# Kernel tuning notes

Measured on AMD Instinct MI355X. Metric: run time of the kernel, lower is better.

Reference implementation:

```python
import jax, jax.numpy as jnp
import numpy as np

K = 9
SIGMA = 4.0
RADIUS = 16  # round(4*sigma)
IMAGE_SHAPE = (256, 256)


def _gaussian_kernel_1d():
    i = jnp.arange(2 * RADIUS + 1, dtype=jnp.float32) - RADIUS
    g = jnp.exp(-(i ** 2) / (2.0 * SIGMA ** 2))
    return g / jnp.sum(g)


def _gaussian_blur(x):
    # x: [b, H, W, 1]; separable Gaussian blur, reflect-101 borders (cv2 default)
    g = _gaussian_kernel_1d()
    xp = jnp.pad(x, ((0, 0), (RADIUS, RADIUS), (RADIUS, RADIUS), (0, 0)), mode='reflect')
    dn = ('NHWC', 'HWIO', 'NHWC')
    kv = g.reshape(2 * RADIUS + 1, 1, 1, 1)  # vertical pass
    kh = g.reshape(1, 2 * RADIUS + 1, 1, 1)  # horizontal pass
    y = jax.lax.conv_general_dilated(xp, kv, (1, 1), 'VALID', dimension_numbers=dn)
    y = jax.lax.conv_general_dilated(y, kh, (1, 1), 'VALID', dimension_numbers=dn)
    return y


def setup_inputs() -> dict:
    key = jax.random.key(0)
    k1, k2 = jax.random.split(key)
    inputs = jax.random.normal(k1, (8, 32, 32, 512), dtype=jnp.float32)
    feature_vector = jax.random.normal(k2, (16384, 512), dtype=jnp.float32)
    return {"inputs": inputs, "feature_vector": feature_vector}


def reference(inputs, feature_vector):
    b, h, w, c = inputs.shape
    feat = inputs.reshape(b * h * w, c)
    # pairwise euclidean distances: [b*h*w, N]
    d2 = (jnp.sum(feat ** 2, axis=-1, keepdims=True)
          + jnp.sum(feature_vector ** 2, axis=-1)[None, :]
          - 2.0 * feat @ feature_vector.T)
    dist = jnp.sqrt(jnp.maximum(d2, 0.0))
    # k smallest distances, ascending (equivalent to tf.sort(...)[..., :k])
    neg_topk, _ = jax.lax.top_k(-dist, K)
    score = -neg_topk  # [b*h*w, K], ascending
    mask = score[:, 0].reshape(b, h, w, 1)
    score = score.reshape(b, h * w, K)
    # patch with maximal nearest-neighbor distance
    idx = jnp.argmax(score[..., 0], axis=-1)  # [b]
    conf = jnp.take_along_axis(score, idx[:, None, None], axis=1)[:, 0, :]  # [b, K]
    exp_conf = jnp.exp(conf)
    weight = 1.0 - jnp.max(exp_conf, axis=-1) / jnp.sum(exp_conf, axis=-1)
    score_out = (jnp.max(score[..., 0], axis=-1) * weight)[:, None]  # [b, 1]
    mask = jax.image.resize(mask, (b, *IMAGE_SHAPE, 1), method='bilinear', antialias=False)
    mask = _gaussian_blur(mask)
    return score_out, mask
```

## Files before the change

kernel.cpp:

```cpp
#include <hip/hip_runtime.h>

typedef __attribute__((ext_vector_type(8))) short bf16x8;
typedef __attribute__((ext_vector_type(4))) float f32x4;

static constexpr int M = 8192;
static constexpr int N = 16384;
static constexpr int K = 512;
static constexpr int BM = 256;
static constexpr int BN = 256;
static constexpr int RBLK = M / BM;
static constexpr int CBLK = N / BN;
static constexpr int BMs = 128;
static constexpr int BKs = 64;
static constexpr int KCHUNKS_S = K / BKs;
static constexpr int NGROUPS_S = 8;
static constexpr int GROUP_N_S = N / NGROUPS_S;
static constexpr int NTILES_S = GROUP_N_S / 128;
static constexpr float F_INF = 3.0e38f;

__device__ __forceinline__ unsigned short f2bf(float f) {
    unsigned int u = __float_as_uint(f);
    return (unsigned short)((u + 0x7fffu + ((u >> 16) & 1u)) >> 16);
}

__device__ __forceinline__ void gl_lds16(const void* g, void* l) {
    __builtin_amdgcn_global_load_lds(
        (const __attribute__((address_space(1))) unsigned int*)g,
        (__attribute__((address_space(3))) unsigned int*)l, 16, 0, 0);
}

__global__ void k_prep(const float* __restrict__ Q, const float* __restrict__ F,
                       unsigned short* __restrict__ Qb, unsigned short* __restrict__ Fb,
                       float* __restrict__ qn, float* __restrict__ fn) {
    int wid = blockIdx.x * 4 + (threadIdx.x >> 6);
    int lane = threadIdx.x & 63;
    bool isQ = wid < M;
    const float* src = isQ ? (Q + (size_t)wid * K) : (F + (size_t)(wid - M) * K);
    unsigned short* dst = isQ ? (Qb + (size_t)wid * K) : (Fb + (size_t)(wid - M) * K);
    const float4* p = reinterpret_cast<const float4*>(src) + lane * 2;
    float4 a = p[0], b = p[1];
    float s = a.x*a.x + a.y*a.y + a.z*a.z + a.w*a.w
            + b.x*b.x + b.y*b.y + b.z*b.z + b.w*b.w;
    bf16x8 v;
    v[0]=(short)f2bf(a.x); v[1]=(short)f2bf(a.y); v[2]=(short)f2bf(a.z); v[3]=(short)f2bf(a.w);
    v[4]=(short)f2bf(b.x); v[5]=(short)f2bf(b.y); v[6]=(short)f2bf(b.z); v[7]=(short)f2bf(b.w);
    *reinterpret_cast<bf16x8*>(dst + lane * 8) = v;
    #pragma unroll
    for (int d = 1; d < 64; d <<= 1) s += __shfl_xor(s, d);
    if (lane == 0) { if (isQ) qn[wid] = s; else fn[wid - M] = s; }
}

__global__ void k_norms(const float* __restrict__ Q, const float* __restrict__ F,
                        float* __restrict__ qn, float* __restrict__ fn) {
    int wid = blockIdx.x * 4 + (threadIdx.x >> 6);
    int lane = threadIdx.x & 63;
    const float* src = (wid < M) ? (Q + (size_t)wid * K) : (F + (size_t)(wid - M) * K);
    const float4* p = reinterpret_cast<const float4*>(src) + lane * 2;
    float4 a = p[0], b = p[1];
    float s = a.x*a.x + a.y*a.y + a.z*a.z + a.w*a.w
            + b.x*b.x + b.y*b.y + b.z*b.z + b.w*b.w;
    #pragma unroll
    for (int d = 1; d < 64; d <<= 1) s += __shfl_xor(s, d);
    if (lane == 0) { if (wid < M) qn[wid] = s; else fn[wid - M] = s; }
}

__global__ __launch_bounds__(512, 1)
void k_mingemm9(const unsigned short* __restrict__ Qb, const unsigned short* __restrict__ Fb,
                const float* __restrict__ qn, const float* __restrict__ fn,
                float* __restrict__ pv, unsigned int* __restrict__ pi) {
    __shared__ unsigned short As[2][2][8192];
    __shared__ unsigned short Bs[2][2][8192];
    __shared__ float redv[256][4];
    __shared__ unsigned int redi[256][4];

    const int tid = threadIdx.x;
    const int lane = tid & 63;
    const int wave = tid >> 6;
    const int wr = wave >> 2;
    const int wc = wave & 3;
    const int l15 = lane & 15, l4 = lane >> 4, l7 = lane & 7;
    const int r3 = lane >> 3;
    const int g8 = (lane & 7) ^ r3;

    const int wg = blockIdx.x;
    const int x = wg & 7, q = wg >> 3;
    const int c_blk = x * 8 + (q & 7);
    const int r_blk = q >> 3;
    const int row0 = r_blk * BM;
    const int col0 = c_blk * BN;

#define STAGE_A(t, hh) do {                                                        \
    _Pragma("unroll")                                                              \
    for (int i = 0; i < 2; ++i)                                                    \
        gl_lds16(Qb + (size_t)(row0 + (hh)*128 + i*64 + wave*8 + r3) * K           \
                    + (t)*64 + g8*8,                                               \
                 &As[(t)&1][hh][(i*64 + wave*8) * 64]);                            \
} while (0)
#define STAGE_B(t, hh) do {                                                        \
    _Pragma("unroll")                                                              \
    for (int i = 0; i < 2; ++i)                                                    \
        gl_lds16(Fb + (size_t)(col0 + (hh)*128 + i*64 + wave*8 + r3) * K           \
                    + (t)*64 + g8*8,                                               \
                 &Bs[(t)&1][hh][(i*64 + wave*8) * 64]);                            \
} while (0)

    f32x4 acc[8][4];
    #pragma unroll
    for (int a = 0; a < 8; ++a)
        #pragma unroll
        for (int b = 0; b < 4; ++b) acc[a][b] = f32x4{0.f, 0.f, 0.f, 0.f};

    bf16x8 afr[4][2], bfr[4][2];

#define PHASE(t, s, STMT, VMN) do {                                                \
    if ((s) == 0) {                                                                \
        _Pragma("unroll")                                                          \
        for (int f = 0; f < 4; ++f)                                                \
            _Pragma("unroll")                                                      \
            for (int ks = 0; ks < 2; ++ks)                                         \
                afr[f][ks] = *reinterpret_cast<const bf16x8*>(                     \
                    &As[(t)&1][wr][(f*16 + l15)*64 + (((ks*4 + l4) ^ l7))*8]);     \
        _Pragma("unroll")                                                          \
        for (int f = 0; f < 2; ++f)                                                \
            _Pragma("unroll")                                                      \
            for (int ks = 0; ks < 2; ++ks)                                         \
                bfr[f][ks] = *reinterpret_cast<const bf16x8*>(                     \
                    &Bs[(t)&1][0][(wc*32 + f*16 + l15)*64 + (((ks*4 + l4) ^ l7))*8]); \
    } else if ((s) == 1) {                                                         \
        _Pragma("unroll")                                                          \
        for (int f = 0; f < 2; ++f)                                                \
            _Pragma("unroll")                                                      \
            for (int ks = 0; ks < 2; ++ks)                                         \
                bfr[2 + f][ks] = *reinterpret_cast<const bf16x8*>(                 \
                    &Bs[(t)&1][1][(wc*32 + f*16 + l15)*64 + (((ks*4 + l4) ^ l7))*8]); \
    } else if ((s) == 2) {                                                         \
        _Pragma("unroll")                                                          \
        for (int f = 0; f < 4; ++f)                                                \
            _Pragma("unroll")                                                      \
            for (int ks = 0; ks < 2; ++ks)                                         \
                afr[f][ks] = *reinterpret_cast<const bf16x8*>(                     \
                    &As[(t)&1][wr][((f+4)*16 + l15)*64 + (((ks*4 + l4) ^ l7))*8]); \
    }                                                                              \
    STMT;                                                                          \
    __builtin_amdgcn_s_setprio(1);                                                 \
    {                                                                              \
        const int AB = ((s) >= 2) ? 4 : 0;                                         \
        const int FJ = ((s) & 1) ? 2 : 0;                                          \
        _Pragma("unroll")                                                          \
        for (int f = 0; f < 4; ++f)                                                \
            _Pragma("unroll")                                                      \
            for (int j2 = 0; j2 < 2; ++j2)                                         \
                _Pragma("unroll")                                                  \
                for (int ks = 0; ks < 2; ++ks)                                     \
                    acc[AB + f][FJ + j2] = __builtin_amdgcn_mfma_f32_16x16x32_bf16(\
                        afr[f][ks], bfr[FJ + j2][ks], acc[AB + f][FJ + j2], 0,0,0);\
    }                                                                              \
    __builtin_amdgcn_s_setprio(0);                                                 \
    asm volatile("s_waitcnt vmcnt(" #VMN ")" ::: "memory");                        \
    __builtin_amdgcn_s_barrier();                                                  \
    __builtin_amdgcn_sched_barrier(0);                                             \
} while (0)

    STAGE_B(0, 0); STAGE_B(0, 1); STAGE_A(0, 0); STAGE_A(0, 1);
    STAGE_B(1, 0); STAGE_B(1, 1); STAGE_A(1, 0);
    asm volatile("s_waitcnt vmcnt(6)" ::: "memory");
    __builtin_amdgcn_s_barrier();
    __builtin_amdgcn_sched_barrier(0);

#define ITER(T)                                        \
    PHASE(T,     0, STAGE_A((T)+1, 1), 6);             \
    PHASE(T,     1, STAGE_B((T)+2, 0), 6);             \
    PHASE(T,     2, STAGE_B((T)+2, 1), 6);             \
    PHASE(T,     3, STAGE_A((T)+2, 0), 6);             \
    PHASE((T)+1, 0, STAGE_A((T)+2, 1), 6);             \
    PHASE((T)+1, 1, STAGE_B((T)+3, 0), 6);             \
    PHASE((T)+1, 2, STAGE_B((T)+3, 1), 6);             \
    PHASE((T)+1, 3, STAGE_A((T)+3, 0), 6);

    ITER(0)
    ITER(2)
    ITER(4)
    PHASE(6, 0, STAGE_A(7, 1), 6);
    PHASE(6, 1, (void)0, 6);
    PHASE(6, 2, (void)0, 6);
    PHASE(6, 3, (void)0, 0);
    PHASE(7, 0, (void)0, 0);
    PHASE(7, 1, (void)0, 0);
    PHASE(7, 2, (void)0, 0);
    PHASE(7, 3, (void)0, 0);
#undef ITER
#undef PHASE
#undef STAGE_A
#undef STAGE_B

    float fnv[4];
    int colg[4];
    #pragma unroll
    for (int fj = 0; fj < 4; ++fj) {
        colg[fj] = col0 + (fj < 2 ? wc*32 + fj*16 : 128 + wc*32 + (fj - 2)*16) + l15;
        fnv[fj] = fn[colg[fj]];
    }
    #pragma unroll
    for (int fi = 0; fi < 8; ++fi) {
        #pragma unroll
        for (int j = 0; j < 4; ++j) {
            int rloc = wr*128 + fi*16 + l4*4 + j;
            float qv = qn[row0 + rloc];
            float v = F_INF; unsigned int ix = 0;
            #pragma unroll
            for (int fj = 0; fj < 4; ++fj) {
                float d2 = qv + fnv[fj] - 2.0f * acc[fi][fj][j];
                if (d2 < v) { v = d2; ix = (unsigned int)colg[fj]; }
            }
            #pragma unroll
            for (int d = 1; d < 16; d <<= 1) {
                float ov = __shfl_xor(v, d);
                unsigned int oi = (unsigned int)__shfl_xor((int)ix, d);
                if (ov < v) { v = ov; ix = oi; }
            }
            if (l15 == 0) { redv[rloc][wc] = v; redi[rloc][wc] = ix; }
        }
    }
    __syncthreads();
    if (tid < BM) {
        float v = redv[tid][0]; unsigned int ix = redi[tid][0];
        #pragma unroll
        for (int w2 = 1; w2 < 4; ++w2) {
            float ov = redv[tid][w2];
            if (ov < v) { v = ov; ix = redi[tid][w2]; }
        }
        pv[(size_t)(row0 + tid) * CBLK + c_blk] = v;
        pi[(size_t)(row0 + tid) * CBLK + c_blk] = ix;
    }
}

__global__ __launch_bounds__(256, 2)
void k_mingemm_cast(const float* __restrict__ Q, const float* __restrict__ F,
                    const float* __restrict__ qn, const float* __restrict__ fn,
                    float* __restrict__ pv, unsigned int* __restrict__ pi) {
    __shared__ unsigned short As[BMs * BKs];
    __shared__ unsigned short Bs[BMs * BKs];
    __shared__ float qn_t[BMs];
    __shared__ float fn_t[BMs];

    const int tid = threadIdx.x;
    const int lane = tid & 63;
    const int wave = tid >> 6;
    const int wr = wave >> 1, wc = wave & 1;
    const int l15 = lane & 15, l4 = lane >> 4;

    const int row0 = blockIdx.x * BMs;
    const int gbase = blockIdx.y * GROUP_N_S;

    const int srow = tid >> 3;
    const int p8 = tid & 7;
    const int g8 = p8 ^ (srow & 7);
    const float* pA[4];
    const float* pB[4];
    int dstOff[4];
    #pragma unroll
    for (int i = 0; i < 4; ++i) {
        int r = i * 32 + srow;
        pA[i] = Q + (size_t)(row0 + r) * K + g8 * 8;
        pB[i] = F + (size_t)(gbase + r) * K + g8 * 8;
        dstOff[i] = r * BKs + p8 * 8;
    }

    float mval[4][4];
    unsigned int midx[4][4];
    float qnv[4][4];
    #pragma unroll
    for (int a = 0; a < 4; ++a)
        #pragma unroll
        for (int b = 0; b < 4; ++b) { mval[a][b] = F_INF; midx[a][b] = 0; qnv[a][b] = 0.f; }

    for (int nt = 0; nt < NTILES_S; ++nt) {
        f32x4 acc[4][4];
        #pragma unroll
        for (int a = 0; a < 4; ++a)
            #pragma unroll
            for (int b = 0; b < 4; ++b) acc[a][b] = f32x4{0.f, 0.f, 0.f, 0.f};

        for (int kc = 0; kc < KCHUNKS_S; ++kc) {
            __syncthreads();
            #pragma unroll
            for (int i = 0; i < 4; ++i) {
                const float4* sa = reinterpret_cast<const float4*>(pA[i] + kc * BKs);
                float4 xa = sa[0], ya = sa[1];
                const float4* sb = reinterpret_cast<const float4*>(pB[i] + nt * (128 * K) + kc * BKs);
                float4 xb = sb[0], yb = sb[1];
                bf16x8 va, vb;
                va[0]=(short)f2bf(xa.x); va[1]=(short)f2bf(xa.y); va[2]=(short)f2bf(xa.z); va[3]=(short)f2bf(xa.w);
                va[4]=(short)f2bf(ya.x); va[5]=(short)f2bf(ya.y); va[6]=(short)f2bf(ya.z); va[7]=(short)f2bf(ya.w);
                vb[0]=(short)f2bf(xb.x); vb[1]=(short)f2bf(xb.y); vb[2]=(short)f2bf(xb.z); vb[3]=(short)f2bf(xb.w);
                vb[4]=(short)f2bf(yb.x); vb[5]=(short)f2bf(yb.y); vb[6]=(short)f2bf(yb.z); vb[7]=(short)f2bf(yb.w);
                *reinterpret_cast<bf16x8*>(&As[dstOff[i]]) = va;
                *reinterpret_cast<bf16x8*>(&Bs[dstOff[i]]) = vb;
            }
            if (kc == 0) {
                if (nt == 0 && tid < BMs) qn_t[tid] = qn[row0 + tid];
                if (tid < 128) fn_t[tid] = fn[gbase + nt * 128 + tid];
            }
            __syncthreads();
            if (nt == 0 && kc == 0) {
                #pragma unroll
                for (int fi = 0; fi < 4; ++fi)
                    #pragma unroll
                    for (int j = 0; j < 4; ++j)
                        qnv[fi][j] = qn_t[wr*64 + fi*16 + l4*4 + j];
            }
            #pragma unroll
            for (int ks = 0; ks < 2; ++ks) {
                const int gidx = ks * 4 + l4;
                bf16x8 af[4], bfv[4];
                #pragma unroll
                for (int fi = 0; fi < 4; ++fi) {
                    int r = wr*64 + fi*16 + l15;
                    int pg = gidx ^ (r & 7);
                    af[fi] = *reinterpret_cast<const bf16x8*>(&As[r*BKs + pg*8]);
                }
                #pragma unroll
                for (int fj = 0; fj < 4; ++fj) {
                    int r = wc*64 + fj*16 + l15;
                    int pg = gidx ^ (r & 7);
                    bfv[fj] = *reinterpret_cast<const bf16x8*>(&Bs[r*BKs + pg*8]);
                }
                #pragma unroll
                for (int fi = 0; fi < 4; ++fi)
                    #pragma unroll
                    for (int fj = 0; fj < 4; ++fj)
                        acc[fi][fj] = __builtin_amdgcn_mfma_f32_16x16x32_bf16(
                            af[fi], bfv[fj], acc[fi][fj], 0, 0, 0);
            }
        }
        const int colb = gbase + nt * 128 + wc * 64;
        float fnv[4];
        #pragma unroll
        for (int fj = 0; fj < 4; ++fj) fnv[fj] = fn_t[wc*64 + fj*16 + l15];
        #pragma unroll
        for (int fi = 0; fi < 4; ++fi) {
            #pragma unroll
            for (int j = 0; j < 4; ++j) {
                float qv = qnv[fi][j];
                #pragma unroll
                for (int fj = 0; fj < 4; ++fj) {
                    float d2 = qv + fnv[fj] - 2.0f * acc[fi][fj][j];
                    if (d2 < mval[fi][j]) {
                        mval[fi][j] = d2;
                        midx[fi][j] = (unsigned int)(colb + fj*16 + l15);
                    }
                }
            }
        }
    }
    #pragma unroll
    for (int fi = 0; fi < 4; ++fi) {
        #pragma unroll
        for (int j = 0; j < 4; ++j) {
            float v = mval[fi][j];
            unsigned int ix = midx[fi][j];
            #pragma unroll
            for (int d = 1; d < 16; d <<= 1) {
                float ov = __shfl_xor(v, d);
                unsigned int oi = (unsigned int)__shfl_xor((int)ix, d);
                if (ov < v) { v = ov; ix = oi; }
            }
            if (l15 == 0) {
                int rg = row0 + wr*64 + fi*16 + l4*4 + j;
                int pidx = rg * 16 + blockIdx.y * 2 + wc;
                pv[pidx] = v;
                pi[pidx] = ix;
            }
        }
    }
}

__global__ void k_refine(const float* __restrict__ Q, const float* __restrict__ F,
                         const float* __restrict__ pv, const unsigned int* __restrict__ pi,
                         float* __restrict__ minD, int PS) {
    int row = blockIdx.x * 4 + (threadIdx.x >> 6);
    int lane = threadIdx.x & 63;
    float v = F_INF; unsigned int ix = 0;
    for (int t = lane; t < PS; t += 64) {
        float nv = pv[(size_t)row*PS + t];
        if (nv < v) { v = nv; ix = pi[(size_t)row*PS + t]; }
    }
    #pragma unroll
    for (int d = 1; d < 64; d <<= 1) {
        float ov = __shfl_xor(v, d);
        unsigned int oi = (unsigned int)__shfl_xor((int)ix, d);
        if (ov < v) { v = ov; ix = oi; }
    }
    const float4* q = reinterpret_cast<const float4*>(Q + (size_t)row * K) + lane*2;
    const float4* f = reinterpret_cast<const float4*>(F + (size_t)ix * K) + lane*2;
    float4 a0 = q[0], a1 = q[1], b0 = f[0], b1 = f[1];
    float s = 0.f, dx;
    dx = a0.x-b0.x; s += dx*dx;  dx = a0.y-b0.y; s += dx*dx;
    dx = a0.z-b0.z; s += dx*dx;  dx = a0.w-b0.w; s += dx*dx;
    dx = a1.x-b1.x; s += dx*dx;  dx = a1.y-b1.y; s += dx*dx;
    dx = a1.z-b1.z; s += dx*dx;  dx = a1.w-b1.w; s += dx*dx;
    #pragma unroll
    for (int d = 1; d < 64; d <<= 1) s += __shfl_xor(s, d);
    if (lane == 0) minD[row] = sqrtf(s);
}

__global__ void k_argmax(const float* __restrict__ minD, unsigned int* __restrict__ sel) {
    __shared__ float sv[256];
    __shared__ int si[256];
    int b = blockIdx.x, tid = threadIdx.x;
    float bv = -F_INF; int bi = 0;
    for (int p = tid; p < 1024; p += 256) {
        float v = minD[b*1024 + p];
        if (v > bv) { bv = v; bi = p; }
    }
    sv[tid] = bv; si[tid] = bi;
    __syncthreads();
    for (int s = 128; s > 0; s >>= 1) {
        if (tid < s) {
            if (sv[tid+s] > sv[tid] || (sv[tid+s] == sv[tid] && si[tid+s] < si[tid])) {
                sv[tid] = sv[tid+s]; si[tid] = si[tid+s];
            }
        }
        __syncthreads();
    }
    if (tid == 0) sel[b] = (unsigned int)(b*1024 + si[0]);
}

__global__ void k_dist8(const float* __restrict__ Q, const float* __restrict__ F,
                        const unsigned int* __restrict__ sel, float* __restrict__ d2all) {
    __shared__ float qs[8][512];
    int tid = threadIdx.x;
    int lane = tid & 63, wave = tid >> 6;
    for (int i = tid; i < 8*512; i += 256) {
        int b = i >> 9;
        qs[b][i & 511] = Q[(size_t)sel[b] * K + (i & 511)];
    }
    __syncthreads();
    int base = blockIdx.x * 128 + wave * 32;
    for (int r = 0; r < 32; ++r) {
        int row = base + r;
        const float4* fp = reinterpret_cast<const float4*>(F + (size_t)row * K) + lane*2;
        float4 f0 = fp[0], f1 = fp[1];
        float fv[8] = {f0.x,f0.y,f0.z,f0.w,f1.x,f1.y,f1.z,f1.w};
        float accb[8];
        #pragma unroll
        for (int b = 0; b < 8; ++b) {
            float s = 0.f;
            #pragma unroll
            for (int e = 0; e < 8; ++e) {
                float d = fv[e] - qs[b][lane*8 + e];
                s += d * d;
            }
            accb[b] = s;
        }
        #pragma unroll
        for (int d = 1; d < 64; d <<= 1)
            #pragma unroll
            for (int b = 0; b < 8; ++b) accb[b] += __shfl_xor(accb[b], d);
        if (lane == 0) {
            #pragma unroll
            for (int b = 0; b < 8; ++b) d2all[b * N + row] = accb[b];
        }
    }
}

__global__ void k_sel9(const float* __restrict__ d2all, float* __restrict__ out) {
    __shared__ float sv[256 * 10];
    int b = blockIdx.x, tid = threadIdx.x;
    float v[9];
    #pragma unroll
    for (int i = 0; i < 9; ++i) v[i] = F_INF;
    for (int i = tid; i < N; i += 256) {
        float x = d2all[b * N + i];
        #pragma unroll
        for (int s = 0; s < 9; ++s) {
            float lo = fminf(v[s], x), hi = fmaxf(v[s], x);
            v[s] = lo; x = hi;
        }
    }
    #pragma unroll
    for (int i = 0; i < 9; ++i) sv[tid*10 + i] = v[i];
    sv[tid*10 + 9] = F_INF;
    __syncthreads();
    for (int s = 128; s > 0; s >>= 1) {
        if (tid < s) {
            int ia = 1, ib = 1;
            float av = sv[tid*10], bv = sv[(tid+s)*10];
            float c[9];
            #pragma unroll
            for (int k = 0; k < 9; ++k) {
                bool ta = av <= bv;
                c[k] = ta ? av : bv;
                float na = sv[tid*10 + ia], nb = sv[(tid+s)*10 + ib];
                if (ta) { av = na; ++ia; } else { bv = nb; ++ib; }
            }
            #pragma unroll
            for (int k = 0; k < 9; ++k) sv[tid*10 + k] = c[k];
        }
        __syncthreads();
    }
    if (tid == 0) {
        float c[9];
        #pragma unroll
        for (int i = 0; i < 9; ++i) c[i] = sqrtf(fmaxf(sv[i], 0.f));
        float S = 0.f;
        #pragma unroll
        for (int i = 0; i < 9; ++i) S += expf(c[i] - c[8]);
        out[b] = c[0] * (1.f - 1.f / S);
    }
}

__global__ void k_top9(const float* __restrict__ Q, const float* __restrict__ F,
                       const unsigned int* __restrict__ sel, float* __restrict__ part9) {
    __shared__ float qs[512];
    __shared__ float dist[2048];
    __shared__ float rv[256];
    __shared__ int ri[256];
    int b = blockIdx.x >> 3, g = blockIdx.x & 7;
    int tid = threadIdx.x;
    unsigned int srow = sel[b];
    if (tid < 128)
        reinterpret_cast<float4*>(qs)[tid] =
            reinterpret_cast<const float4*>(Q + (size_t)srow * K)[tid];
    __syncthreads();
    #pragma unroll
    for (int e = 0; e < 8; ++e) {
        int fl = tid + 256*e;
        const float* fp = F + (size_t)(g*2048 + fl) * K;
        float s = 0.f;
        for (int k = 0; k < 512; k += 4) {
            float4 fv4 = *reinterpret_cast<const float4*>(fp + k);
            float d0 = qs[k]   - fv4.x;
            float d1 = qs[k+1] - fv4.y;
            float d2 = qs[k+2] - fv4.z;
            float d3 = qs[k+3] - fv4.w;
            s += d0*d0 + d1*d1 + d2*d2 + d3*d3;
        }
        dist[fl] = s;
    }
    __syncthreads();
    for (int it = 0; it < 9; ++it) {
        float lv = F_INF; int li = 0;
        #pragma unroll
        for (int e = 0; e < 8; ++e) {
            int idx = tid + 256*e;
            float v = dist[idx];
            if (v < lv) { lv = v; li = idx; }
        }
        rv[tid] = lv; ri[tid] = li;
        __syncthreads();
        for (int s = 128; s > 0; s >>= 1) {
            if (tid < s && rv[tid+s] < rv[tid]) { rv[tid] = rv[tid+s]; ri[tid] = ri[tid+s]; }
            __syncthreads();
        }
        if (tid == 0) {
            part9[(b*8+g)*9 + it] = rv[0];
            dist[ri[0]] = F_INF;
        }
        __syncthreads();
    }
}

__global__ void k_final(const float* __restrict__ part9, float* __restrict__ out) {
    int b = threadIdx.x;
    if (b >= 8) return;
    float arr[9];
    #pragma unroll
    for (int i = 0; i < 9; ++i) arr[i] = F_INF;
    for (int g = 0; g < 8; ++g)
        for (int i = 0; i < 9; ++i) {
            float v = part9[(b*8+g)*9 + i];
            #pragma unroll
            for (int s = 0; s < 9; ++s) {
                float lo = fminf(arr[s], v), hi = fmaxf(arr[s], v);
                arr[s] = lo; v = hi;
            }
        }
    float c[9];
    #pragma unroll
    for (int i = 0; i < 9; ++i) c[i] = sqrtf(fmaxf(arr[i], 0.f));
    float c8 = c[8], S = 0.f;
    #pragma unroll
    for (int i = 0; i < 9; ++i) S += expf(c[i] - c8);
    float w = 1.f - 1.f / S;
    out[b] = c[0] * w;
}

__global__ void k_wmat(float* __restrict__ W) {
    int idx = blockIdx.x * 256 + threadIdx.x;
    int o = idx >> 5, j = idx & 31;
    float gsum = 0.f;
    #pragma unroll
    for (int u = 0; u < 33; ++u) { float d = (float)(u - 16); gsum += expf(-d*d * (1.f/32.f)); }
    float acc = 0.f;
    for (int u = 0; u < 33; ++u) {
        float d = (float)(u - 16);
        float gu = expf(-d*d * (1.f/32.f));
        int y = o + u - 16;
        y = y < 0 ? -y : (y > 255 ? 510 - y : y);
        float xin = ((float)y + 0.5f) * 0.125f - 0.5f;
        float j0f = floorf(xin);
        int j0 = (int)j0f;
        float wfr = xin - j0f;
        float r;
        if (j0 < 0) r = (j == 0) ? 1.f : 0.f;
        else if (j0 >= 31) r = (j == 31) ? 1.f : 0.f;
        else r = (j == j0) ? (1.f - wfr) : ((j == j0 + 1) ? wfr : 0.f);
        acc += gu * r;
    }
    W[idx] = acc / gsum;
}

__global__ void k_mask(const float* __restrict__ minD, const float* __restrict__ W,
                       float* __restrict__ outm) {
    __shared__ float Ms[1024];
    __shared__ float Ws[8192];
    __shared__ float Ts[8192];
    int b = blockIdx.x, tid = threadIdx.x;
    for (int i = tid; i < 1024; i += 256) Ms[i] = minD[b*1024 + i];
    for (int i = tid; i < 8192; i += 256) Ws[i] = W[i];
    __syncthreads();
    {
        int o = tid;
        float wrow[32];
        #pragma unroll
        for (int i = 0; i < 32; ++i) wrow[i] = Ws[o*32 + i];
        for (int j = 0; j < 32; ++j) {
            float s = 0.f;
            #pragma unroll
            for (int i = 0; i < 32; ++i) s += wrow[i] * Ms[i*32 + j];
            Ts[o*32 + j] = s;
        }
    }
    __syncthreads();
    {
        int p = tid;
        float wp[32];
        #pragma unroll
        for (int j = 0; j < 32; ++j) wp[j] = Ws[p*32 + j];
        float* dst = outm + (size_t)b * 65536;
        for (int o = 0; o < 256; ++o) {
            float s = 0.f;
            #pragma unroll
            for (int j = 0; j < 32; ++j) s += Ts[o*32 + j] * wp[j];
            dst[o*256 + p] = s;
        }
    }
}

extern "C" void kernel_launch(void* const* d_in, const int* in_sizes, int n_in,
                              void* d_out, int out_size, void* d_ws, size_t ws_size,
                              hipStream_t stream) {
    const float* Q = (const float*)d_in[0];
    const float* F = (const float*)d_in[1];
    float* out = (float*)d_out;

    const size_t smallFloats = (size_t)8192*64*2 + 8192 + 8 + 576 + (size_t)8*N + 8192 + 16384 + 8192;
    const size_t REQ = smallFloats*4 + (size_t)M*K*2 + (size_t)N*K*2;
    const bool fast = ws_size >= REQ;

    float* ws = (float*)d_ws;
    float* pv = ws;
    unsigned int* pi = (unsigned int*)(pv + 8192*64);
    float* minD = (float*)(pi + 8192*64);
    unsigned int* sel = (unsigned int*)(minD + 8192);
    float* part9 = (float*)(sel + 8);
    float* d2all = part9 + 576;
    float* qn = d2all + (size_t)8*N;
    float* fn = qn + 8192;
    float* W  = fn + 16384;
    unsigned short* Qb = (unsigned short*)(W + 8192);
    unsigned short* Fb = Qb + (size_t)M*K;

    k_wmat <<<dim3(32), 256, 0, stream>>>(W);
    if (fast) {
        k_prep <<<dim3((M + N) / 4), 256, 0, stream>>>(Q, F, Qb, Fb, qn, fn);
        k_mingemm9<<<dim3(RBLK * CBLK), 512, 0, stream>>>(Qb, Fb, qn, fn, pv, pi);
        k_refine<<<dim3(M / 4), 256, 0, stream>>>(Q, F, pv, pi, minD, 64);
        k_argmax<<<dim3(8), 256, 0, stream>>>(minD, sel);
        k_dist8<<<dim3(N / 128), 256, 0, stream>>>(Q, F, sel, d2all);
        k_sel9 <<<dim3(8), 256, 0, stream>>>(d2all, out);
    } else {
        k_norms<<<dim3((M + N) / 4), 256, 0, stream>>>(Q, F, qn, fn);
        k_mingemm_cast<<<dim3(M / BMs, NGROUPS_S), 256, 0, stream>>>(Q, F, qn, fn, pv, pi);
        k_refine<<<dim3(M / 4), 256, 0, stream>>>(Q, F, pv, pi, minD, 16);
        k_argmax<<<dim3(8), 256, 0, stream>>>(minD, sel);
        k_top9 <<<dim3(64), 256, 0, stream>>>(Q, F, sel, part9);
        k_final<<<dim3(1), 64, 0, stream>>>(part9, out);
    }
    k_mask <<<dim3(8), 256, 0, stream>>>(minD, W, out + 8);
}
```

Before: 335.1 us.

## Make min-GEMM persistent over eight column tiles with continuous pipelined staging

Replaces the grid of 2048 one-tile workgroups with 256 persistent workgroups. Each covers one 256-row block and walks eight consecutive 256-column tiles, with the double-buffered global-to-LDS pipeline running across tile boundaries. After each tile it folds the accumulators into per-row minima and writes them to the same partial-min layout as before. This is meant to remove per-workgroup launch, prologue and pipeline-drain costs and keep the A rows resident in L2. In exchange the fold step stalls the MFMA pipeline between tiles, and there are exactly 256 workgroups, which leaves load balance tied to the CU count.

New measurement: 361.6 us. 7.9% more time.

```diff
diff --git a/kernel.cpp b/kernel.cpp
--- a/kernel.cpp
+++ b/kernel.cpp
@@ -7,9 +7,6 @@
 static constexpr int N = 16384;
 static constexpr int K = 512;
 static constexpr int BM = 256;
-static constexpr int BN = 256;
-static constexpr int RBLK = M / BM;
-static constexpr int CBLK = N / BN;
 static constexpr int BMs = 128;
 static constexpr int BKs = 64;
 static constexpr int KCHUNKS_S = K / BKs;
@@ -65,9 +62,9 @@
 }
 
 __global__ __launch_bounds__(512, 1)
-void k_mingemm9(const unsigned short* __restrict__ Qb, const unsigned short* __restrict__ Fb,
-                const float* __restrict__ qn, const float* __restrict__ fn,
-                float* __restrict__ pv, unsigned int* __restrict__ pi) {
+void k_mingemm10(const unsigned short* __restrict__ Qb, const unsigned short* __restrict__ Fb,
+                 const float* __restrict__ qn, const float* __restrict__ fn,
+                 float* __restrict__ pv, unsigned int* __restrict__ pi) {
     __shared__ unsigned short As[2][2][8192];
     __shared__ unsigned short Bs[2][2][8192];
     __shared__ float redv[256][4];
@@ -83,25 +80,24 @@
     const int g8 = (lane & 7) ^ r3;
 
     const int wg = blockIdx.x;
-    const int x = wg & 7, q = wg >> 3;
-    const int c_blk = x * 8 + (q & 7);
-    const int r_blk = q >> 3;
-    const int row0 = r_blk * BM;
-    const int col0 = c_blk * BN;
-
-#define STAGE_A(t, hh) do {                                                        \
+    const int cg = wg & 7;
+    const int rb = wg >> 3;
+    const int row0 = rb * BM;
+    const int colP = cg * 2048;
+
+#define STAGE_A(g, hh) do {                                                        \
     _Pragma("unroll")                                                              \
     for (int i = 0; i < 2; ++i)                                                    \
         gl_lds16(Qb + (size_t)(row0 + (hh)*128 + i*64 + wave*8 + r3) * K           \
-                    + (t)*64 + g8*8,                                               \
-                 &As[(t)&1][hh][(i*64 + wave*8) * 64]);                            \
+                    + ((g)&7)*64 + g8*8,                                           \
+                 &As[(g)&1][hh][(i*64 + wave*8) * 64]);                            \
 } while (0)
-#define STAGE_B(t, hh) do {                                                        \
+#define STAGE_B(g, hh) do {                                                        \
     _Pragma("unroll")                                                              \
     for (int i = 0; i < 2; ++i)                                                    \
-        gl_lds16(Fb + (size_t)(col0 + (hh)*128 + i*64 + wave*8 + r3) * K           \
-                    + (t)*64 + g8*8,                                               \
-                 &Bs[(t)&1][hh][(i*64 + wave*8) * 64]);                            \
+        gl_lds16(Fb + (size_t)(colP + ((g)>>3)*256 + (hh)*128 + i*64 + wave*8 + r3) * K \
+                    + ((g)&7)*64 + g8*8,                                           \
+                 &Bs[(g)&1][hh][(i*64 + wave*8) * 64]);                            \
 } while (0)
 
     f32x4 acc[8][4];
@@ -161,77 +157,82 @@
     __builtin_amdgcn_sched_barrier(0);                                             \
 } while (0)
 
+    auto fold = [&](int nt) {
+        const int colbase = colP + nt * 256;
+        float fnv[4];
+        int colg[4];
+        #pragma unroll
+        for (int fj = 0; fj < 4; ++fj) {
+            colg[fj] = colbase + (fj < 2 ? wc*32 + fj*16 : 128 + wc*32 + (fj - 2)*16) + l15;
+            fnv[fj] = fn[colg[fj]];
+        }
+        #pragma unroll
+        for (int fi = 0; fi < 8; ++fi) {
+            #pragma unroll
+            for (int j = 0; j < 4; ++j) {
+                int rloc = wr*128 + fi*16 + l4*4 + j;
+                float qv = qn[row0 + rloc];
+                float v = F_INF; unsigned int ix = 0;
+                #pragma unroll
+                for (int fj = 0; fj < 4; ++fj) {
+                    float d2 = qv + fnv[fj] - 2.0f * acc[fi][fj][j];
+                    if (d2 < v) { v = d2; ix = (unsigned int)colg[fj]; }
+                }
+                #pragma unroll
+                for (int d = 1; d < 16; d <<= 1) {
+                    float ov = __shfl_xor(v, d);
+                    unsigned int oi = (unsigned int)__shfl_xor((int)ix, d);
+                    if (ov < v) { v = ov; ix = oi; }
+                }
+                if (l15 == 0) { redv[rloc][wc] = v; redi[rloc][wc] = ix; }
+            }
+        }
+        asm volatile("s_waitcnt lgkmcnt(0)" ::: "memory");
+        __builtin_amdgcn_sched_barrier(0);
+        __builtin_amdgcn_s_barrier();
+        if (tid < BM) {
+            float v = redv[tid][0]; unsigned int ix = redi[tid][0];
+            #pragma unroll
+            for (int w2 = 1; w2 < 4; ++w2) {
+                float ov = redv[tid][w2];
+                if (ov < v) { v = ov; ix = redi[tid][w2]; }
+            }
+            pv[(size_t)(row0 + tid) * 64 + cg*8 + nt] = v;
+            pi[(size_t)(row0 + tid) * 64 + cg*8 + nt] = ix;
+        }
+        __builtin_amdgcn_s_barrier();
+        __builtin_amdgcn_sched_barrier(0);
+        #pragma unroll
+        for (int a = 0; a < 8; ++a)
+            #pragma unroll
+            for (int b = 0; b < 4; ++b) acc[a][b] = f32x4{0.f, 0.f, 0.f, 0.f};
+    };
+
     STAGE_B(0, 0); STAGE_B(0, 1); STAGE_A(0, 0); STAGE_A(0, 1);
     STAGE_B(1, 0); STAGE_B(1, 1); STAGE_A(1, 0);
     asm volatile("s_waitcnt vmcnt(6)" ::: "memory");
     __builtin_amdgcn_s_barrier();
     __builtin_amdgcn_sched_barrier(0);
 
-#define ITER(T)                                        \
-    PHASE(T,     0, STAGE_A((T)+1, 1), 6);             \
-    PHASE(T,     1, STAGE_B((T)+2, 0), 6);             \
-    PHASE(T,     2, STAGE_B((T)+2, 1), 6);             \
-    PHASE(T,     3, STAGE_A((T)+2, 0), 6);             \
-    PHASE((T)+1, 0, STAGE_A((T)+2, 1), 6);             \
-    PHASE((T)+1, 1, STAGE_B((T)+3, 0), 6);             \
-    PHASE((T)+1, 2, STAGE_B((T)+3, 1), 6);             \
-    PHASE((T)+1, 3, STAGE_A((T)+3, 0), 6);
-
-    ITER(0)
-    ITER(2)
-    ITER(4)
-    PHASE(6, 0, STAGE_A(7, 1), 6);
-    PHASE(6, 1, (void)0, 6);
-    PHASE(6, 2, (void)0, 6);
-    PHASE(6, 3, (void)0, 0);
-    PHASE(7, 0, (void)0, 0);
-    PHASE(7, 1, (void)0, 0);
-    PHASE(7, 2, (void)0, 0);
-    PHASE(7, 3, (void)0, 0);
-#undef ITER
+    for (int g = 0; g < 62; ++g) {
+        PHASE(g, 0, STAGE_A(g + 1, 1), 6);
+        PHASE(g, 1, STAGE_B(g + 2, 0), 6);
+        PHASE(g, 2, STAGE_B(g + 2, 1), 6);
+        PHASE(g, 3, STAGE_A(g + 2, 0), 6);
+        if ((g & 7) == 7) fold(g >> 3);
+    }
+    PHASE(62, 0, STAGE_A(63, 1), 6);
+    PHASE(62, 1, (void)0, 6);
+    PHASE(62, 2, (void)0, 6);
+    PHASE(62, 3, (void)0, 0);
+    PHASE(63, 0, (void)0, 0);
+    PHASE(63, 1, (void)0, 0);
+    PHASE(63, 2, (void)0, 0);
+    PHASE(63, 3, (void)0, 0);
+    fold(7);
 #undef PHASE
 #undef STAGE_A
 #undef STAGE_B
-
-    float fnv[4];
-    int colg[4];
-    #pragma unroll
-    for (int fj = 0; fj < 4; ++fj) {
-        colg[fj] = col0 + (fj < 2 ? wc*32 + fj*16 : 128 + wc*32 + (fj - 2)*16) + l15;
-        fnv[fj] = fn[colg[fj]];
-    }
-    #pragma unroll
-    for (int fi = 0; fi < 8; ++fi) {
-        #pragma unroll
-        for (int j = 0; j < 4; ++j) {
-            int rloc = wr*128 + fi*16 + l4*4 + j;
-            float qv = qn[row0 + rloc];
-            float v = F_INF; unsigned int ix = 0;
-            #pragma unroll
-            for (int fj = 0; fj < 4; ++fj) {
-                float d2 = qv + fnv[fj] - 2.0f * acc[fi][fj][j];
-                if (d2 < v) { v = d2; ix = (unsigned int)colg[fj]; }
-            }
-            #pragma unroll
-            for (int d = 1; d < 16; d <<= 1) {
-                float ov = __shfl_xor(v, d);
-                unsigned int oi = (unsigned int)__shfl_xor((int)ix, d);
-                if (ov < v) { v = ov; ix = oi; }
-            }
-            if (l15 == 0) { redv[rloc][wc] = v; redi[rloc][wc] = ix; }
-        }
-    }
-    __syncthreads();
-    if (tid < BM) {
-        float v = redv[tid][0]; unsigned int ix = redi[tid][0];
-        #pragma unroll
-        for (int w2 = 1; w2 < 4; ++w2) {
-            float ov = redv[tid][w2];
-            if (ov < v) { v = ov; ix = redi[tid][w2]; }
-        }
-        pv[(size_t)(row0 + tid) * CBLK + c_blk] = v;
-        pi[(size_t)(row0 + tid) * CBLK + c_blk] = ix;
-    }
 }
 
 __global__ __launch_bounds__(256, 2)
@@ -675,7 +676,7 @@
     k_wmat <<<dim3(32), 256, 0, stream>>>(W);
     if (fast) {
         k_prep <<<dim3((M + N) / 4), 256, 0, stream>>>(Q, F, Qb, Fb, qn, fn);
-        k_mingemm9<<<dim3(RBLK * CBLK), 512, 0, stream>>>(Qb, Fb, qn, fn, pv, pi);
+        k_mingemm10<<<dim3(256), 512, 0, stream>>>(Qb, Fb, qn, fn, pv, pi);
         k_refine<<<dim3(M / 4), 256, 0, stream>>>(Q, F, pv, pi, minD, 64);
         k_argmax<<<dim3(8), 256, 0, stream>>>(minD, sel);
         k_dist8<<<dim3(N / 128), 256, 0, stream>>>(Q, F, sel, d2all);
```
